# Performance work log

Measured on AMD Instinct MI355X. Metric: run time of the kernel, lower is better.

## Reference

```python
import jax, jax.numpy as jnp
import numpy as np

MARGIN_1 = 0.3
ALPHA_1 = 0.5
EPS = 1e-12
NEG = -1e30


def setup_inputs() -> dict:
    key = jax.random.key(0)
    batch_size = 128
    d = 2048
    N = 2 * batch_size
    feature = jax.random.normal(key, (N, d), dtype=jnp.float32)
    # PK-sampled ids: 32 identities x 4 instances, same ids in both modality halves
    num_ids = 32
    ids = jnp.repeat(jnp.arange(num_ids, dtype=jnp.int32), batch_size // num_ids)
    targets = jnp.concatenate([ids, ids])  # (N,)
    return {"feature": feature, "targets": targets}


def reference(feature, targets):
    N = feature.shape[0]
    # modality indicator: first half 0, second half 1 (self.sub)
    sub = jnp.arange(N) >= (N // 2)
    G = feature @ feature.T  # (N, N) gram matrix, symmetric

    pos_mat = targets[:, None] == targets[None, :]   # is_pos per anchor row
    intra_mat = sub[:, None] == sub[None, :]          # intra-modality per anchor row

    def msm(col_mask):
        # row-wise softmax of G restricted to columns in col_mask, zeros elsewhere
        logits = jnp.where(col_mask[None, :], G, NEG)
        return jax.nn.softmax(logits, axis=-1) * col_mask[None, :].astype(G.dtype)

    def trans(row_mask, col_mask):
        # ab: (intra rows -> cross cols) transition probs; ba: (cross -> intra)
        ab = msm(col_mask)
        ba = msm(row_mask)  # G symmetric, so softmax over row_mask cols == match.T softmax
        t = ab @ ba  # round-trip transition probability, valid on row_mask x row_mask
        return jnp.sqrt(jnp.clip(t, EPS))

    def masked_mean(v, m):
        mf = m.astype(v.dtype)
        w = mf[:, None] * mf[None, :]
        return jnp.sum(v * w) / jnp.sum(w)

    def per_anchor(is_pos, intra):
        is_neg = ~is_pos
        cross = ~intra
        mpi = is_pos & intra
        mpc = is_pos & cross
        mni = is_neg & intra
        mnc = is_neg & cross
        t_pos = trans(mpi, mpc)
        t_neg = trans(mni, mnc)
        loss_ap = masked_mean(jnp.clip(t_neg + (MARGIN_1 - ALPHA_1), 0.0, None), mni)
        loss_an = masked_mean(jnp.clip(ALPHA_1 - t_pos, 0.0, None), mpi)
        return loss_ap + loss_an

    loss = jnp.mean(jax.vmap(per_anchor)(pos_mat, intra_mat))

    # hard-mining accuracy over euclidean distance matrix
    sq = jnp.sum(feature * feature, axis=1)
    dist = jnp.sqrt(jnp.clip(sq[:, None] + sq[None, :] - 2.0 * G, EPS))
    dist_ap = jnp.max(jnp.where(pos_mat, dist, -jnp.inf), axis=1)
    dist_an = jnp.min(jnp.where(~pos_mat, dist, jnp.inf), axis=1)
    correct = jnp.sum((dist_an >= dist_ap).astype(jnp.int32))
    return loss, correct
```

## Files before the change

### kernel.cpp

```cpp
#include <hip/hip_runtime.h>

#define EPSF 1e-12f

__device__ __forceinline__ unsigned short f2bf(float f) {
  unsigned int u = __float_as_uint(f);
  unsigned int r = u + 0x7fffu + ((u >> 16) & 1u);
  return (unsigned short)(r >> 16);
}
#define BFLO(u) __uint_as_float((u) << 16)
#define BFHI(u) __uint_as_float((u) & 0xffff0000u)

__global__ void gemm_tile(const float* __restrict__ F, float* __restrict__ Gout,
                          int n, int d, int kchunk) {
  __shared__ float As[64][36];
  __shared__ float Bs[64][36];
  const int tid = threadIdx.x;
  const int bx = blockIdx.x, by = blockIdx.y, kz = blockIdx.z;
  const int ty = tid >> 4, tx = tid & 15;
  const int lrow = tid >> 2;
  const int lcol = (tid & 3) * 8;
  const float* Ap = F + (size_t)(bx * 64 + lrow) * d + (size_t)kz * kchunk + lcol;
  const float* Bp = F + (size_t)(by * 64 + lrow) * d + (size_t)kz * kchunk + lcol;
  float acc[4][4];
  for (int r = 0; r < 4; r++)
    for (int c = 0; c < 4; c++) acc[r][c] = 0.0f;

  for (int ks = 0; ks < kchunk; ks += 32) {
    float4 a0 = *(const float4*)(Ap + ks);
    float4 a1 = *(const float4*)(Ap + ks + 4);
    float4 b0 = *(const float4*)(Bp + ks);
    float4 b1 = *(const float4*)(Bp + ks + 4);
    __syncthreads();
    *(float4*)&As[lrow][lcol]     = a0;
    *(float4*)&As[lrow][lcol + 4] = a1;
    *(float4*)&Bs[lrow][lcol]     = b0;
    *(float4*)&Bs[lrow][lcol + 4] = b1;
    __syncthreads();
#pragma unroll
    for (int kk = 0; kk < 32; kk += 4) {
      float4 av[4], bv[4];
#pragma unroll
      for (int r = 0; r < 4; r++) av[r] = *(const float4*)&As[ty + 16 * r][kk];
#pragma unroll
      for (int c = 0; c < 4; c++) bv[c] = *(const float4*)&Bs[tx + 16 * c][kk];
#pragma unroll
      for (int r = 0; r < 4; r++) {
        float4 A = av[r];
#pragma unroll
        for (int c = 0; c < 4; c++) {
          float4 B = bv[c];
          acc[r][c] += A.x * B.x + A.y * B.y + A.z * B.z + A.w * B.w;
        }
      }
    }
  }
  float* Gs = Gout + (size_t)kz * n * n;
#pragma unroll
  for (int r = 0; r < 4; r++)
#pragma unroll
    for (int c = 0; c < 4; c++)
      Gs[(size_t)(bx * 64 + ty + 16 * r) * n + (by * 64 + tx + 16 * c)] =
          acc[r][c];
}

__global__ void reduce_slices(const float* __restrict__ Gp,
                              float* __restrict__ G, int nn, int nslices) {
  int e = (blockIdx.x * 256 + threadIdx.x) * 4;
  if (e < nn) {
    float4 s = *(const float4*)(Gp + e);
    for (int k = 1; k < nslices; k++) {
      float4 t = *(const float4*)(Gp + (size_t)k * nn + e);
      s.x += t.x; s.y += t.y; s.z += t.z; s.w += t.w;
    }
    *(float4*)(G + e) = s;
  }
}

__global__ void stats_kernel(const float* __restrict__ G,
                             const int* __restrict__ targets,
                             float* __restrict__ LSEtab,
                             float* __restrict__ flags, int n) {
  __shared__ float bins[4][33];
  __shared__ int tg[256];
  __shared__ float diag[256];
  const int tid = threadIdx.x;
  const int lane = tid & 63;
  const int w = tid >> 6;
  tg[tid] = targets[tid];
  diag[tid] = G[(size_t)tid * (n + 1)];
  if (tid < 128) bins[tid >> 5][tid & 31] = 0.0f;
  __syncthreads();

  const int r = blockIdx.x * 4 + w;
  const int nhalf = n >> 1;
  const int opp0 = (r < nhalf) ? nhalf : 0;
  const int myid = tg[r];
  const float sqr = diag[r];

  float4 v = *(const float4*)(G + (size_t)r * n + lane * 4);
  float gv[4] = {v.x, v.y, v.z, v.w};

  float dap = -1e30f, dan = 1e30f;
#pragma unroll
  for (int q = 0; q < 4; q++) {
    int j = lane * 4 + q;
    float dist = sqrtf(fmaxf(sqr + diag[j] - 2.0f * gv[q], EPSF));
    if (tg[j] == myid) dap = fmaxf(dap, dist);
    else               dan = fminf(dan, dist);
  }
#pragma unroll
  for (int off = 32; off; off >>= 1) {
    dap = fmaxf(dap, __shfl_xor(dap, off));
    dan = fminf(dan, __shfl_xor(dan, off));
  }
  if (lane == 0) flags[r] = (dan >= dap) ? 1.0f : 0.0f;

  float mx = -1e30f;
#pragma unroll
  for (int q = 0; q < 4; q++) {
    int j = lane * 4 + q;
    if (j >= opp0 && j < opp0 + nhalf) mx = fmaxf(mx, gv[q]);
  }
#pragma unroll
  for (int off = 32; off; off >>= 1) mx = fmaxf(mx, __shfl_xor(mx, off));

#pragma unroll
  for (int q = 0; q < 4; q++) {
    int j = lane * 4 + q;
    if (j >= opp0 && j < opp0 + nhalf)
      atomicAdd(&bins[w][tg[j]], __expf(gv[q] - mx));
  }
  __syncthreads();

  if (lane < 32) {
    float b = bins[w][lane];
    float lv = __shfl_up(b, 1, 32);
    if (lane == 0) lv = 0.0f;
#pragma unroll
    for (int off = 1; off < 32; off <<= 1) {
      float t = __shfl_up(lv, off, 32);
      if (lane >= off) lv += t;
    }
    float rv = __shfl_down(b, 1, 32);
    if (lane == 31) rv = 0.0f;
#pragma unroll
    for (int off = 1; off < 32; off <<= 1) {
      float t = __shfl_down(rv, off, 32);
      if (lane + off < 32) rv += t;
    }
    float excl = fmaxf(lv + rv, 1e-37f);
    LSEtab[(size_t)r * 32 + lane] = mx + __logf(excl);
  }
}

__global__ __launch_bounds__(256, 2) void TransitionLoss_30666066494151_kernel(
    const float* __restrict__ G, const int* __restrict__ targets,
    const float* __restrict__ LSEtab, float* __restrict__ lsp,
    float* __restrict__ lan, float* __restrict__ cnts, int n) {
  __shared__ unsigned short W[128][136];
  __shared__ int tg[256];
  __shared__ int maskA[128], maskB[128];
  __shared__ float Ri[128], Cl[128];
  __shared__ float SMRAW[16][17];
  __shared__ float SP[16][17], SQ[16][17];
  __shared__ float red[256];
  __shared__ int Plist[16], Qlist[16];
  __shared__ int ctrP, ctrQ;

  const int tid = threadIdx.x;
  const int cls = blockIdx.x;
  const int part = blockIdx.y;
  const int nhalf = n >> 1;
  const int myid = cls & 31;
  const int hA = cls >> 5;
  const int rowA0 = hA * nhalf;
  const int colB0 = nhalf - rowA0;

  tg[tid] = targets[tid];
  if (tid == 0) { ctrP = 0; ctrQ = 0; }
  __syncthreads();

  if (tid < 128) {
    maskA[tid] = (tg[rowA0 + tid] != myid) ? 1 : 0;
    Ri[tid] = LSEtab[(size_t)(rowA0 + tid) * 32 + myid];
  } else {
    maskB[tid - 128] = (tg[colB0 + tid - 128] != myid) ? 1 : 0;
    Cl[tid - 128] = LSEtab[(size_t)(colB0 + tid - 128) * 32 + myid];
  }
  if (tg[tid] == myid) {
    int inAhalf = (((tid >= nhalf) ? 1 : 0) == hA) ? 1 : 0;
    if (inAhalf) { int k = atomicAdd(&ctrP, 1); if (k < 16) Plist[k] = tid; }
    else         { int k = atomicAdd(&ctrQ, 1); if (k < 16) Qlist[k] = tid; }
  }
  __syncthreads();
  const int nP = min(ctrP, 16), nQ = min(ctrQ, 16);

#pragma unroll
  for (int k8 = 0; k8 < 2; k8++) {
    float4 g[8];
#pragma unroll
    for (int u = 0; u < 8; u++) {
      int e4 = tid + 256 * (k8 * 8 + u);
      int i = e4 >> 5;
      int l4 = (e4 & 31) << 2;
      g[u] = *(const float4*)(G + (size_t)(rowA0 + i) * n + colB0 + l4);
    }
#pragma unroll
    for (int u = 0; u < 8; u++) {
      int e4 = tid + 256 * (k8 * 8 + u);
      int i = e4 >> 5;
      int l4 = (e4 & 31) << 2;
      float rih = 0.5f * Ri[i];
      int ma = maskA[i];
      float w0 = (ma && maskB[l4 + 0]) ? __expf(g[u].x - rih - 0.5f * Cl[l4 + 0]) : 0.0f;
      float w1 = (ma && maskB[l4 + 1]) ? __expf(g[u].y - rih - 0.5f * Cl[l4 + 1]) : 0.0f;
      float w2 = (ma && maskB[l4 + 2]) ? __expf(g[u].z - rih - 0.5f * Cl[l4 + 2]) : 0.0f;
      float w3 = (ma && maskB[l4 + 3]) ? __expf(g[u].w - rih - 0.5f * Cl[l4 + 3]) : 0.0f;
      uint2 packed;
      packed.x = (unsigned)f2bf(w0) | ((unsigned)f2bf(w1) << 16);
      packed.y = (unsigned)f2bf(w2) | ((unsigned)f2bf(w3) << 16);
      *(uint2*)&W[i][l4] = packed;
    }
  }

  if (part == 0) {
    int p = tid >> 4, q = tid & 15;
    float v = 0.0f;
    if (p < nP && q < nQ) v = G[(size_t)Plist[p] * n + Qlist[q]];
    SMRAW[p][q] = v;
  }
  __syncthreads();

  const int i0 = part * 16;
  const int ty = tid >> 4, tx = tid & 15;
  const float riA = Ri[i0 + ty];
  float acc[8];
#pragma unroll
  for (int c = 0; c < 8; c++) acc[c] = 0.0f;

  for (int kk = 0; kk < 128; kk += 8) {
    uint4 ar = *(const uint4*)&W[i0 + ty][kk];
    uint4 br[8];
#pragma unroll
    for (int c = 0; c < 8; c++) br[c] = *(const uint4*)&W[tx + 16 * c][kk];
    float a0 = BFLO(ar.x), a1 = BFHI(ar.x), a2 = BFLO(ar.y), a3 = BFHI(ar.y);
    float a4 = BFLO(ar.z), a5 = BFHI(ar.z), a6 = BFLO(ar.w), a7 = BFHI(ar.w);
#pragma unroll
    for (int c = 0; c < 8; c++) {
      acc[c] += a0 * BFLO(br[c].x) + a1 * BFHI(br[c].x) +
                a2 * BFLO(br[c].y) + a3 * BFHI(br[c].y) +
                a4 * BFLO(br[c].z) + a5 * BFHI(br[c].z) +
                a6 * BFLO(br[c].w) + a7 * BFHI(br[c].w);
    }
  }

  float lsum = 0.0f;
#pragma unroll
  for (int c = 0; c < 8; c++) {
    int j = tx + 16 * c;
    float t = __expf(0.5f * (Ri[j] - riA)) * acc[c];
    lsum += fmaxf(sqrtf(fmaxf(t, EPSF)) - 0.2f, 0.0f);
  }
  red[tid] = lsum;
  __syncthreads();
  for (int s2 = 128; s2 > 0; s2 >>= 1) {
    if (tid < s2) red[tid] += red[tid + s2];
    __syncthreads();
  }
  if (tid == 0) lsp[cls * 8 + part] = red[0];

  if (part == 0) {
    __syncthreads();
    red[tid] = (tid < 128) ? (float)maskA[tid] : 0.0f;
    __syncthreads();
    for (int s2 = 128; s2 > 0; s2 >>= 1) {
      if (tid < s2) red[tid] += red[tid + s2];
      __syncthreads();
    }
    if (tid == 0) { cnts[cls * 2 + 0] = red[0]; cnts[cls * 2 + 1] = (float)nP; }

    if (tid < nP) {
      float mx = -1e30f;
      for (int q = 0; q < nQ; q++) mx = fmaxf(mx, SMRAW[tid][q]);
      float s = 0.0f;
      for (int q = 0; q < nQ; q++) s += __expf(SMRAW[tid][q] - mx);
      for (int q = 0; q < nQ; q++) SP[tid][q] = __expf(SMRAW[tid][q] - mx) / s;
    }
    if (tid >= 64 && tid < 64 + nQ) {
      int q = tid - 64;
      float mx = -1e30f;
      for (int p = 0; p < nP; p++) mx = fmaxf(mx, SMRAW[p][q]);
      float s = 0.0f;
      for (int p = 0; p < nP; p++) s += __expf(SMRAW[p][q] - mx);
      for (int p = 0; p < nP; p++) SQ[q][p] = __expf(SMRAW[p][q] - mx) / s;
    }
    __syncthreads();
    float lv = 0.0f;
    if (tid < nP * nP) {
      int i = tid / nP, j = tid - i * nP;
      float t = 0.0f;
      for (int l = 0; l < nQ; l++) t += SP[i][l] * SQ[l][j];
      lv = fmaxf(0.5f - sqrtf(fmaxf(t, EPSF)), 0.0f);
    }
    red[tid] = lv;
    __syncthreads();
    for (int s2 = 128; s2 > 0; s2 >>= 1) {
      if (tid < s2) red[tid] += red[tid + s2];
      __syncthreads();
    }
    if (tid == 0) lan[cls] = red[0];
  }
}

__global__ void final_reduce(const float* __restrict__ lsp,
                             const float* __restrict__ lan,
                             const float* __restrict__ cnts,
                             const float* __restrict__ flags,
                             float* __restrict__ out, int n) {
  __shared__ float rl[256], rf[256];
  const int tid = threadIdx.x;
  float lv = 0.0f;
  if (tid < 64) {
    float nA = cnts[tid * 2 + 0];
    float nP = cnts[tid * 2 + 1];
    if (nP > 0.5f && nA > 0.5f) {
      float s = 0.0f;
      for (int p = 0; p < 8; p++) s += lsp[tid * 8 + p];
      float lc = s / (nA * nA) + lan[tid] / (nP * nP);
      lv = nP * lc;
    }
  }
  rl[tid] = lv;
  rf[tid] = flags[tid];
  __syncthreads();
  for (int s2 = 128; s2 > 0; s2 >>= 1) {
    if (tid < s2) { rl[tid] += rl[tid + s2]; rf[tid] += rf[tid + s2]; }
    __syncthreads();
  }
  if (tid == 0) {
    out[0] = rl[0] / (float)n;
    out[1] = rf[0];
  }
}

extern "C" void kernel_launch(void* const* d_in, const int* in_sizes, int n_in,
                              void* d_out, int out_size, void* d_ws,
                              size_t ws_size, hipStream_t stream) {
  const float* feature = (const float*)d_in[0];
  const int* targets = (const int*)d_in[1];
  const int n = in_sizes[1];
  const int d = in_sizes[0] / n;
  const int nn = n * n;
  const size_t small = 512 + 64 + 128 + 256 + (size_t)n * 32;

  int S = 1;
  if (ws_size >= (small + nn + (size_t)16 * nn) * sizeof(float)) S = 16;
  else if (ws_size >= (small + nn + (size_t)4 * nn) * sizeof(float)) S = 4;

  float* ws = (float*)d_ws;
  float* lsp = ws;
  float* lan = lsp + 512;
  float* cnts = lan + 64;
  float* flags = cnts + 128;
  float* LSEtab = flags + 256;
  float* G = LSEtab + (size_t)n * 32;
  float* Gp = (S > 1) ? (G + nn) : G;
  float* out = (float*)d_out;

  dim3 gg(n / 64, n / 64, S);
  gemm_tile<<<gg, 256, 0, stream>>>(feature, Gp, n, d, d / S);
  if (S > 1)
    reduce_slices<<<(nn + 1023) / 1024, 256, 0, stream>>>(Gp, G, nn, S);

  stats_kernel<<<n / 4, 256, 0, stream>>>(G, targets, LSEtab, flags, n);

  dim3 gc(64, 8);
  TransitionLoss_30666066494151_kernel<<<gc, 256, 0, stream>>>(
      G, targets, LSEtab, lsp, lan, cnts, n);

  final_reduce<<<1, 256, 0, stream>>>(lsp, lan, cnts, flags, out, n);
}
```

Measured before the change: 56.27 us.

## Fuse split-K reduction into stats kernel and use MFMA for transition GEMM

The separate reduce_slices launch is removed: stats_kernel now sums the split-K partial Gram slices itself and writes the reduced G rows while computing distances and LSE stats. The 128x128 bf16 round-trip product in the loss kernel moves from scalar FMA split over 8 blocks per class to MFMA 16x16x32 bf16 instructions, with one block per class doing the full tile, which drops the y-dimension of the grid and the partial-sum buffer. The LSE table is transposed so the loss kernel reads it contiguously. This saves one launch and a pass over G in exchange for less block parallelism in the loss kernel (64 blocks instead of 512).

```diff
diff --git a/kernel.cpp b/kernel.cpp
--- a/kernel.cpp
+++ b/kernel.cpp
@@ -1,14 +1,15 @@
 #include <hip/hip_runtime.h>
 
 #define EPSF 1e-12f
+
+typedef short bf16x8 __attribute__((ext_vector_type(8)));
+typedef float f32x4 __attribute__((ext_vector_type(4)));
 
 __device__ __forceinline__ unsigned short f2bf(float f) {
   unsigned int u = __float_as_uint(f);
   unsigned int r = u + 0x7fffu + ((u >> 16) & 1u);
   return (unsigned short)(r >> 16);
 }
-#define BFLO(u) __uint_as_float((u) << 16)
-#define BFHI(u) __uint_as_float((u) & 0xffff0000u)
 
 __global__ void gemm_tile(const float* __restrict__ F, float* __restrict__ Gout,
                           int n, int d, int kchunk) {
@@ -63,31 +64,24 @@
           acc[r][c];
 }
 
-__global__ void reduce_slices(const float* __restrict__ Gp,
-                              float* __restrict__ G, int nn, int nslices) {
-  int e = (blockIdx.x * 256 + threadIdx.x) * 4;
-  if (e < nn) {
-    float4 s = *(const float4*)(Gp + e);
-    for (int k = 1; k < nslices; k++) {
-      float4 t = *(const float4*)(Gp + (size_t)k * nn + e);
-      s.x += t.x; s.y += t.y; s.z += t.z; s.w += t.w;
-    }
-    *(float4*)(G + e) = s;
-  }
-}
-
-__global__ void stats_kernel(const float* __restrict__ G,
+__global__ void stats_kernel(const float* __restrict__ Gp,
                              const int* __restrict__ targets,
-                             float* __restrict__ LSEtab,
-                             float* __restrict__ flags, int n) {
+                             float* __restrict__ G, float* __restrict__ LSEtab,
+                             float* __restrict__ flags, int n, int S) {
   __shared__ float bins[4][33];
   __shared__ int tg[256];
   __shared__ float diag[256];
   const int tid = threadIdx.x;
   const int lane = tid & 63;
   const int w = tid >> 6;
+  const int nn = n * n;
   tg[tid] = targets[tid];
-  diag[tid] = G[(size_t)tid * (n + 1)];
+  {
+    float s0 = 0.0f;
+    for (int s = 0; s < S; s++)
+      s0 += Gp[(size_t)s * nn + (size_t)tid * (n + 1)];
+    diag[tid] = s0;
+  }
   if (tid < 128) bins[tid >> 5][tid & 31] = 0.0f;
   __syncthreads();
 
@@ -97,7 +91,12 @@
   const int myid = tg[r];
   const float sqr = diag[r];
 
-  float4 v = *(const float4*)(G + (size_t)r * n + lane * 4);
+  float4 v = make_float4(0.f, 0.f, 0.f, 0.f);
+  for (int s = 0; s < S; s++) {
+    float4 t = *(const float4*)(Gp + (size_t)s * nn + (size_t)r * n + lane * 4);
+    v.x += t.x; v.y += t.y; v.z += t.z; v.w += t.w;
+  }
+  *(float4*)(G + (size_t)r * n + lane * 4) = v;
   float gv[4] = {v.x, v.y, v.z, v.w};
 
   float dap = -1e30f, dan = 1e30f;
@@ -149,11 +148,11 @@
       if (lane + off < 32) rv += t;
     }
     float excl = fmaxf(lv + rv, 1e-37f);
-    LSEtab[(size_t)r * 32 + lane] = mx + __logf(excl);
-  }
-}
-
-__global__ __launch_bounds__(256, 2) void TransitionLoss_30666066494151_kernel(
+    LSEtab[(size_t)lane * n + r] = mx + __logf(excl);
+  }
+}
+
+__global__ void TransitionLoss_30666066494151_kernel(
     const float* __restrict__ G, const int* __restrict__ targets,
     const float* __restrict__ LSEtab, float* __restrict__ lsp,
     float* __restrict__ lan, float* __restrict__ cnts, int n) {
@@ -161,15 +160,13 @@
   __shared__ int tg[256];
   __shared__ int maskA[128], maskB[128];
   __shared__ float Ri[128], Cl[128];
-  __shared__ float SMRAW[16][17];
-  __shared__ float SP[16][17], SQ[16][17];
+  __shared__ float SMRAW[16][17], SP[16][17], SQ[16][17];
   __shared__ float red[256];
   __shared__ int Plist[16], Qlist[16];
   __shared__ int ctrP, ctrQ;
 
   const int tid = threadIdx.x;
   const int cls = blockIdx.x;
-  const int part = blockIdx.y;
   const int nhalf = n >> 1;
   const int myid = cls & 31;
   const int hA = cls >> 5;
@@ -182,10 +179,10 @@
 
   if (tid < 128) {
     maskA[tid] = (tg[rowA0 + tid] != myid) ? 1 : 0;
-    Ri[tid] = LSEtab[(size_t)(rowA0 + tid) * 32 + myid];
+    Ri[tid] = LSEtab[(size_t)myid * n + rowA0 + tid];
   } else {
     maskB[tid - 128] = (tg[colB0 + tid - 128] != myid) ? 1 : 0;
-    Cl[tid - 128] = LSEtab[(size_t)(colB0 + tid - 128) * 32 + myid];
+    Cl[tid - 128] = LSEtab[(size_t)myid * n + colB0 + tid - 128];
   }
   if (tg[tid] == myid) {
     int inAhalf = (((tid >= nhalf) ? 1 : 0) == hA) ? 1 : 0;
@@ -223,7 +220,7 @@
     }
   }
 
-  if (part == 0) {
+  {
     int p = tid >> 4, q = tid & 15;
     float v = 0.0f;
     if (p < nP && q < nQ) v = G[(size_t)Plist[p] * n + Qlist[q]];
@@ -231,85 +228,95 @@
   }
   __syncthreads();
 
-  const int i0 = part * 16;
-  const int ty = tid >> 4, tx = tid & 15;
-  const float riA = Ri[i0 + ty];
-  float acc[8];
-#pragma unroll
-  for (int c = 0; c < 8; c++) acc[c] = 0.0f;
-
-  for (int kk = 0; kk < 128; kk += 8) {
-    uint4 ar = *(const uint4*)&W[i0 + ty][kk];
-    uint4 br[8];
-#pragma unroll
-    for (int c = 0; c < 8; c++) br[c] = *(const uint4*)&W[tx + 16 * c][kk];
-    float a0 = BFLO(ar.x), a1 = BFHI(ar.x), a2 = BFLO(ar.y), a3 = BFHI(ar.y);
-    float a4 = BFLO(ar.z), a5 = BFHI(ar.z), a6 = BFLO(ar.w), a7 = BFHI(ar.w);
+  const int lane = tid & 63;
+  const int wv = tid >> 6;
+  const int m16 = lane & 15;
+  const int kh = lane >> 4;
+  f32x4 acc[2][8];
+#pragma unroll
+  for (int r = 0; r < 2; r++)
+#pragma unroll
+    for (int c = 0; c < 8; c++) acc[r][c] = (f32x4){0.f, 0.f, 0.f, 0.f};
+
+#pragma unroll
+  for (int kc = 0; kc < 4; kc++) {
+    const int koff = kc * 32 + kh * 8;
+    bf16x8 bfrag[8];
+#pragma unroll
+    for (int c = 0; c < 8; c++)
+      bfrag[c] = *(const bf16x8*)&W[c * 16 + m16][koff];
+#pragma unroll
+    for (int r = 0; r < 2; r++) {
+      bf16x8 afrag = bfrag[wv * 2 + r];
+#pragma unroll
+      for (int c = 0; c < 8; c++)
+        acc[r][c] = __builtin_amdgcn_mfma_f32_16x16x32_bf16(
+            afrag, bfrag[c], acc[r][c], 0, 0, 0);
+    }
+  }
+
+  float lsum = 0.0f;
+#pragma unroll
+  for (int r = 0; r < 2; r++)
 #pragma unroll
     for (int c = 0; c < 8; c++) {
-      acc[c] += a0 * BFLO(br[c].x) + a1 * BFHI(br[c].x) +
-                a2 * BFLO(br[c].y) + a3 * BFHI(br[c].y) +
-                a4 * BFLO(br[c].z) + a5 * BFHI(br[c].z) +
-                a6 * BFLO(br[c].w) + a7 * BFHI(br[c].w);
-    }
-  }
-
-  float lsum = 0.0f;
-#pragma unroll
-  for (int c = 0; c < 8; c++) {
-    int j = tx + 16 * c;
-    float t = __expf(0.5f * (Ri[j] - riA)) * acc[c];
-    lsum += fmaxf(sqrtf(fmaxf(t, EPSF)) - 0.2f, 0.0f);
-  }
+      f32x4 D = acc[r][c];
+      int jcol = c * 16 + m16;
+      float rj = Ri[jcol];
+#pragma unroll
+      for (int e = 0; e < 4; e++) {
+        int irow = wv * 32 + r * 16 + kh * 4 + e;
+        float t = __expf(0.5f * (rj - Ri[irow])) * D[e];
+        lsum += fmaxf(sqrtf(fmaxf(t, EPSF)) - 0.2f, 0.0f);
+      }
+    }
   red[tid] = lsum;
   __syncthreads();
   for (int s2 = 128; s2 > 0; s2 >>= 1) {
     if (tid < s2) red[tid] += red[tid + s2];
     __syncthreads();
   }
-  if (tid == 0) lsp[cls * 8 + part] = red[0];
-
-  if (part == 0) {
-    __syncthreads();
-    red[tid] = (tid < 128) ? (float)maskA[tid] : 0.0f;
-    __syncthreads();
-    for (int s2 = 128; s2 > 0; s2 >>= 1) {
-      if (tid < s2) red[tid] += red[tid + s2];
-      __syncthreads();
-    }
-    if (tid == 0) { cnts[cls * 2 + 0] = red[0]; cnts[cls * 2 + 1] = (float)nP; }
-
-    if (tid < nP) {
-      float mx = -1e30f;
-      for (int q = 0; q < nQ; q++) mx = fmaxf(mx, SMRAW[tid][q]);
-      float s = 0.0f;
-      for (int q = 0; q < nQ; q++) s += __expf(SMRAW[tid][q] - mx);
-      for (int q = 0; q < nQ; q++) SP[tid][q] = __expf(SMRAW[tid][q] - mx) / s;
-    }
-    if (tid >= 64 && tid < 64 + nQ) {
-      int q = tid - 64;
-      float mx = -1e30f;
-      for (int p = 0; p < nP; p++) mx = fmaxf(mx, SMRAW[p][q]);
-      float s = 0.0f;
-      for (int p = 0; p < nP; p++) s += __expf(SMRAW[p][q] - mx);
-      for (int p = 0; p < nP; p++) SQ[q][p] = __expf(SMRAW[p][q] - mx) / s;
-    }
-    __syncthreads();
-    float lv = 0.0f;
-    if (tid < nP * nP) {
-      int i = tid / nP, j = tid - i * nP;
-      float t = 0.0f;
-      for (int l = 0; l < nQ; l++) t += SP[i][l] * SQ[l][j];
-      lv = fmaxf(0.5f - sqrtf(fmaxf(t, EPSF)), 0.0f);
-    }
-    red[tid] = lv;
-    __syncthreads();
-    for (int s2 = 128; s2 > 0; s2 >>= 1) {
-      if (tid < s2) red[tid] += red[tid + s2];
-      __syncthreads();
-    }
-    if (tid == 0) lan[cls] = red[0];
-  }
+  if (tid == 0) lsp[cls] = red[0];
+
+  __syncthreads();
+  red[tid] = (tid < 128) ? (float)maskA[tid] : 0.0f;
+  __syncthreads();
+  for (int s2 = 128; s2 > 0; s2 >>= 1) {
+    if (tid < s2) red[tid] += red[tid + s2];
+    __syncthreads();
+  }
+  if (tid == 0) { cnts[cls * 2 + 0] = red[0]; cnts[cls * 2 + 1] = (float)nP; }
+
+  if (tid < nP) {
+    float mx = -1e30f;
+    for (int q = 0; q < nQ; q++) mx = fmaxf(mx, SMRAW[tid][q]);
+    float s = 0.0f;
+    for (int q = 0; q < nQ; q++) s += __expf(SMRAW[tid][q] - mx);
+    for (int q = 0; q < nQ; q++) SP[tid][q] = __expf(SMRAW[tid][q] - mx) / s;
+  }
+  if (tid >= 64 && tid < 64 + nQ) {
+    int q = tid - 64;
+    float mx = -1e30f;
+    for (int p = 0; p < nP; p++) mx = fmaxf(mx, SMRAW[p][q]);
+    float s = 0.0f;
+    for (int p = 0; p < nP; p++) s += __expf(SMRAW[p][q] - mx);
+    for (int p = 0; p < nP; p++) SQ[q][p] = __expf(SMRAW[p][q] - mx) / s;
+  }
+  __syncthreads();
+  float lv = 0.0f;
+  if (tid < nP * nP) {
+    int i = tid / nP, j = tid - i * nP;
+    float t = 0.0f;
+    for (int l = 0; l < nQ; l++) t += SP[i][l] * SQ[l][j];
+    lv = fmaxf(0.5f - sqrtf(fmaxf(t, EPSF)), 0.0f);
+  }
+  red[tid] = lv;
+  __syncthreads();
+  for (int s2 = 128; s2 > 0; s2 >>= 1) {
+    if (tid < s2) red[tid] += red[tid + s2];
+    __syncthreads();
+  }
+  if (tid == 0) lan[cls] = red[0];
 }
 
 __global__ void final_reduce(const float* __restrict__ lsp,
@@ -323,12 +330,8 @@
   if (tid < 64) {
     float nA = cnts[tid * 2 + 0];
     float nP = cnts[tid * 2 + 1];
-    if (nP > 0.5f && nA > 0.5f) {
-      float s = 0.0f;
-      for (int p = 0; p < 8; p++) s += lsp[tid * 8 + p];
-      float lc = s / (nA * nA) + lan[tid] / (nP * nP);
-      lv = nP * lc;
-    }
+    if (nP > 0.5f && nA > 0.5f)
+      lv = nP * (lsp[tid] / (nA * nA) + lan[tid] / (nP * nP));
   }
   rl[tid] = lv;
   rf[tid] = flags[tid];
@@ -351,7 +354,7 @@
   const int n = in_sizes[1];
   const int d = in_sizes[0] / n;
   const int nn = n * n;
-  const size_t small = 512 + 64 + 128 + 256 + (size_t)n * 32;
+  const size_t small = 64 + 64 + 128 + 256 + (size_t)n * 32;
 
   int S = 1;
   if (ws_size >= (small + nn + (size_t)16 * nn) * sizeof(float)) S = 16;
@@ -359,7 +362,7 @@
 
   float* ws = (float*)d_ws;
   float* lsp = ws;
-  float* lan = lsp + 512;
+  float* lan = lsp + 64;
   float* cnts = lan + 64;
   float* flags = cnts + 128;
   float* LSEtab = flags + 256;
@@ -369,13 +372,10 @@
 
   dim3 gg(n / 64, n / 64, S);
   gemm_tile<<<gg, 256, 0, stream>>>(feature, Gp, n, d, d / S);
-  if (S > 1)
-    reduce_slices<<<(nn + 1023) / 1024, 256, 0, stream>>>(Gp, G, nn, S);
-
-  stats_kernel<<<n / 4, 256, 0, stream>>>(G, targets, LSEtab, flags, n);
-
-  dim3 gc(64, 8);
-  TransitionLoss_30666066494151_kernel<<<gc, 256, 0, stream>>>(
+
+  stats_kernel<<<n / 4, 256, 0, stream>>>(Gp, targets, G, LSEtab, flags, n, S);
+
+  TransitionLoss_30666066494151_kernel<<<64, 256, 0, stream>>>(
       G, targets, LSEtab, lsp, lan, cnts, n);
 
   final_reduce<<<1, 256, 0, stream>>>(lsp, lan, cnts, flags, out, n);
```

Measured after the change: 62.37 us. 1.11x slower.

## Fuse split-K reduction into stats kernel and final reduce into loss kernel

Applied to the files above, without the earlier changes.

The split-K slice sum moves into stats_kernel, which reads the partial Gram slices, writes the reduced G rows and computes stats in the same pass. The final reduction is folded into the transition-loss kernel through a last-block ticket atomic with thread fences, and the LSE table is transposed so loads in the loss kernel are coalesced. This removes two kernel launches and one full pass over G. It adds a memset of the ticket counter, and diag is now recomputed from the slices by every block.

```diff
diff --git a/kernel.cpp b/kernel.cpp
--- a/kernel.cpp
+++ b/kernel.cpp
@@ -63,31 +63,24 @@
           acc[r][c];
 }
 
-__global__ void reduce_slices(const float* __restrict__ Gp,
-                              float* __restrict__ G, int nn, int nslices) {
-  int e = (blockIdx.x * 256 + threadIdx.x) * 4;
-  if (e < nn) {
-    float4 s = *(const float4*)(Gp + e);
-    for (int k = 1; k < nslices; k++) {
-      float4 t = *(const float4*)(Gp + (size_t)k * nn + e);
-      s.x += t.x; s.y += t.y; s.z += t.z; s.w += t.w;
-    }
-    *(float4*)(G + e) = s;
-  }
-}
-
-__global__ void stats_kernel(const float* __restrict__ G,
+__global__ void stats_kernel(const float* __restrict__ Gp,
                              const int* __restrict__ targets,
-                             float* __restrict__ LSEtab,
-                             float* __restrict__ flags, int n) {
+                             float* __restrict__ G, float* __restrict__ LSEtab,
+                             float* __restrict__ flags, int n, int S) {
   __shared__ float bins[4][33];
   __shared__ int tg[256];
   __shared__ float diag[256];
   const int tid = threadIdx.x;
   const int lane = tid & 63;
   const int w = tid >> 6;
+  const int nn = n * n;
   tg[tid] = targets[tid];
-  diag[tid] = G[(size_t)tid * (n + 1)];
+  {
+    float s0 = 0.0f;
+    for (int s = 0; s < S; s++)
+      s0 += Gp[(size_t)s * nn + (size_t)tid * (n + 1)];
+    diag[tid] = s0;
+  }
   if (tid < 128) bins[tid >> 5][tid & 31] = 0.0f;
   __syncthreads();
 
@@ -97,7 +90,12 @@
   const int myid = tg[r];
   const float sqr = diag[r];
 
-  float4 v = *(const float4*)(G + (size_t)r * n + lane * 4);
+  float4 v = make_float4(0.f, 0.f, 0.f, 0.f);
+  for (int s = 0; s < S; s++) {
+    float4 t = *(const float4*)(Gp + (size_t)s * nn + (size_t)r * n + lane * 4);
+    v.x += t.x; v.y += t.y; v.z += t.z; v.w += t.w;
+  }
+  *(float4*)(G + (size_t)r * n + lane * 4) = v;
   float gv[4] = {v.x, v.y, v.z, v.w};
 
   float dap = -1e30f, dan = 1e30f;
@@ -149,23 +147,26 @@
       if (lane + off < 32) rv += t;
     }
     float excl = fmaxf(lv + rv, 1e-37f);
-    LSEtab[(size_t)r * 32 + lane] = mx + __logf(excl);
+    LSEtab[(size_t)lane * n + r] = mx + __logf(excl);
   }
 }
 
 __global__ __launch_bounds__(256, 2) void TransitionLoss_30666066494151_kernel(
     const float* __restrict__ G, const int* __restrict__ targets,
     const float* __restrict__ LSEtab, float* __restrict__ lsp,
-    float* __restrict__ lan, float* __restrict__ cnts, int n) {
+    float* __restrict__ lan, float* __restrict__ cnts,
+    const float* __restrict__ flags, unsigned* __restrict__ ticket,
+    float* __restrict__ out, int n) {
   __shared__ unsigned short W[128][136];
   __shared__ int tg[256];
   __shared__ int maskA[128], maskB[128];
   __shared__ float Ri[128], Cl[128];
   __shared__ float SMRAW[16][17];
   __shared__ float SP[16][17], SQ[16][17];
-  __shared__ float red[256];
+  __shared__ float red[256], red2[256];
   __shared__ int Plist[16], Qlist[16];
   __shared__ int ctrP, ctrQ;
+  __shared__ int islast;
 
   const int tid = threadIdx.x;
   const int cls = blockIdx.x;
@@ -182,10 +183,10 @@
 
   if (tid < 128) {
     maskA[tid] = (tg[rowA0 + tid] != myid) ? 1 : 0;
-    Ri[tid] = LSEtab[(size_t)(rowA0 + tid) * 32 + myid];
+    Ri[tid] = LSEtab[(size_t)myid * n + rowA0 + tid];
   } else {
     maskB[tid - 128] = (tg[colB0 + tid - 128] != myid) ? 1 : 0;
-    Cl[tid - 128] = LSEtab[(size_t)(colB0 + tid - 128) * 32 + myid];
+    Cl[tid - 128] = LSEtab[(size_t)myid * n + colB0 + tid - 128];
   }
   if (tg[tid] == myid) {
     int inAhalf = (((tid >= nhalf) ? 1 : 0) == hA) ? 1 : 0;
@@ -310,36 +311,37 @@
     }
     if (tid == 0) lan[cls] = red[0];
   }
-}
-
-__global__ void final_reduce(const float* __restrict__ lsp,
-                             const float* __restrict__ lan,
-                             const float* __restrict__ cnts,
-                             const float* __restrict__ flags,
-                             float* __restrict__ out, int n) {
-  __shared__ float rl[256], rf[256];
-  const int tid = threadIdx.x;
-  float lv = 0.0f;
-  if (tid < 64) {
-    float nA = cnts[tid * 2 + 0];
-    float nP = cnts[tid * 2 + 1];
-    if (nP > 0.5f && nA > 0.5f) {
-      float s = 0.0f;
-      for (int p = 0; p < 8; p++) s += lsp[tid * 8 + p];
-      float lc = s / (nA * nA) + lan[tid] / (nP * nP);
-      lv = nP * lc;
-    }
-  }
-  rl[tid] = lv;
-  rf[tid] = flags[tid];
-  __syncthreads();
-  for (int s2 = 128; s2 > 0; s2 >>= 1) {
-    if (tid < s2) { rl[tid] += rl[tid + s2]; rf[tid] += rf[tid + s2]; }
-    __syncthreads();
-  }
+
+  __syncthreads();
   if (tid == 0) {
-    out[0] = rl[0] / (float)n;
-    out[1] = rf[0];
+    __threadfence();
+    unsigned t = atomicAdd(ticket, 1u);
+    islast = (t == gridDim.x * gridDim.y - 1) ? 1 : 0;
+  }
+  __syncthreads();
+  if (islast) {
+    __threadfence();
+    float lv = 0.0f;
+    if (tid < 64) {
+      float nA = cnts[tid * 2 + 0];
+      float nP2 = cnts[tid * 2 + 1];
+      if (nP2 > 0.5f && nA > 0.5f) {
+        float s = 0.0f;
+        for (int p = 0; p < 8; p++) s += lsp[tid * 8 + p];
+        lv = nP2 * (s / (nA * nA) + lan[tid] / (nP2 * nP2));
+      }
+    }
+    red[tid] = lv;
+    red2[tid] = flags[tid];
+    __syncthreads();
+    for (int s2 = 128; s2 > 0; s2 >>= 1) {
+      if (tid < s2) { red[tid] += red[tid + s2]; red2[tid] += red2[tid + s2]; }
+      __syncthreads();
+    }
+    if (tid == 0) {
+      out[0] = red[0] / (float)n;
+      out[1] = red2[0];
+    }
   }
 }
 
@@ -351,14 +353,15 @@
   const int n = in_sizes[1];
   const int d = in_sizes[0] / n;
   const int nn = n * n;
-  const size_t small = 512 + 64 + 128 + 256 + (size_t)n * 32;
+  const size_t smallf = 16 + 512 + 64 + 128 + 256 + (size_t)n * 32;
 
   int S = 1;
-  if (ws_size >= (small + nn + (size_t)16 * nn) * sizeof(float)) S = 16;
-  else if (ws_size >= (small + nn + (size_t)4 * nn) * sizeof(float)) S = 4;
-
-  float* ws = (float*)d_ws;
-  float* lsp = ws;
+  if (ws_size >= (smallf + nn + (size_t)16 * nn) * sizeof(float)) S = 16;
+  else if (ws_size >= (smallf + nn + (size_t)4 * nn) * sizeof(float)) S = 4;
+
+  unsigned* ticket = (unsigned*)d_ws;
+  float* base = (float*)d_ws + 16;
+  float* lsp = base;
   float* lan = lsp + 512;
   float* cnts = lan + 64;
   float* flags = cnts + 128;
@@ -367,16 +370,14 @@
   float* Gp = (S > 1) ? (G + nn) : G;
   float* out = (float*)d_out;
 
+  hipMemsetAsync(d_ws, 0, 16 * sizeof(unsigned), stream);
+
   dim3 gg(n / 64, n / 64, S);
   gemm_tile<<<gg, 256, 0, stream>>>(feature, Gp, n, d, d / S);
-  if (S > 1)
-    reduce_slices<<<(nn + 1023) / 1024, 256, 0, stream>>>(Gp, G, nn, S);
-
-  stats_kernel<<<n / 4, 256, 0, stream>>>(G, targets, LSEtab, flags, n);
+
+  stats_kernel<<<n / 4, 256, 0, stream>>>(Gp, targets, G, LSEtab, flags, n, S);
 
   dim3 gc(64, 8);
   TransitionLoss_30666066494151_kernel<<<gc, 256, 0, stream>>>(
-      G, targets, LSEtab, lsp, lan, cnts, n);
-
-  final_reduce<<<1, 256, 0, stream>>>(lsp, lan, cnts, flags, out, n);
-}
+      G, targets, LSEtab, lsp, lan, cnts, flags, ticket, out, n);
+}
```

Result: slower. 70.58 us (+25.4%).
